# Optimization experiments

Hardware: AMD Instinct MI355X
Metric: run time of the kernel (lower is better)

Reference implementation:

```python
import jax, jax.numpy as jnp
import numpy as np


def _rule_stack(x_q):
    # x_q: [B, 2, 4]; a/b are the two context panels, per attribute column -> [B, 4]
    a = x_q[:, 0, :]
    b = x_q[:, 1, :]
    # 13 fixed rules applied elementwise across the 4 attribute columns -> [B, 4, 13]
    return jnp.stack([
        a,
        b - 2.0, b - 1.0, b + 1.0, b + 2.0,
        a - b, a + b,
        jnp.minimum(a, b), jnp.maximum(a, b),
        b + 2.0, b + 1.0, b - 2.0, b - 1.0,
    ], axis=-1)


def setup_inputs() -> dict:
    key = jax.random.key(0)
    k1, k2, k3, k4 = jax.random.split(key, 4)
    B, Z = 262144, 512
    z = jax.random.normal(k1, (B, Z), dtype=jnp.float32)
    x_q = jax.random.normal(k2, (B, 2, 4), dtype=jnp.float32)
    # rule_encoder: Linear(z_dim -> 4*13)
    W = jax.random.normal(k3, (Z, 52), dtype=jnp.float32) / np.sqrt(Z)
    b = jax.random.normal(k4, (52,), dtype=jnp.float32) * 0.01
    return {"z": z, "x_q": x_q, "W": W, "b": b}


def reference(z, x_q, W, b):
    logits = (z @ W + b).reshape(-1, 4, 13)          # [B, 4, 13]
    rule_probs = jax.nn.softmax(logits, axis=-1)       # [B, 4, 13]
    rules = _rule_stack(x_q)                           # [B, 4, 13]
    y_q = jnp.sum(rules * rule_probs, axis=-1)         # [B, 4]
    return y_q[:, None, :]                             # [B, 1, 4]
```

## Files before the change

kernel.cpp:

```cpp
#include <hip/hip_runtime.h>
#include <stdint.h>

typedef __bf16 bf16_t;
typedef bf16_t bf16x8 __attribute__((ext_vector_type(8)));
typedef float f32x4 __attribute__((ext_vector_type(4)));
typedef uint32_t u32x4 __attribute__((ext_vector_type(4)));
typedef uint16_t u16x8 __attribute__((ext_vector_type(8)));

union FragU { u32x4 u; bf16x8 v; u16x8 s; };

__device__ __forceinline__ uint16_t f2bf_rne(float f) {
  uint32_t u = __float_as_uint(f);
  return (uint16_t)((u + 0x7fffu + ((u >> 16) & 1u)) >> 16);
}
__device__ __forceinline__ float bf2f_bits(uint16_t h) {
  return __uint_as_float(((uint32_t)h) << 16);
}

__global__ __launch_bounds__(256) void pack_w_kernel(
    const float* __restrict__ W, u32x4* __restrict__ wf_hi,
    u32x4* __restrict__ wf_lo) {
  int idx = blockIdx.x * 256 + threadIdx.x;
  if (idx >= 4096) return;
  int lane = idx & 63;
  int nt   = (idx >> 6) & 3;
  int ks   = idx >> 8;
  int n  = nt * 16 + (lane & 15);
  int kb = ks * 32 + (lane >> 4) * 8;
  FragU hi, lo;
#pragma unroll
  for (int j = 0; j < 8; ++j) {
    float w = (n < 52) ? W[(kb + j) * 52 + n] : 0.0f;
    uint16_t h = f2bf_rne(w);
    hi.s[j] = h;
    lo.s[j] = f2bf_rne(w - bf2f_bits(h));
  }
  wf_hi[idx] = hi.u;
  wf_lo[idx] = lo.u;
}

#define MFMA16(a, b, c) __builtin_amdgcn_mfma_f32_16x16x32_bf16((a), (b), (c), 0, 0, 0)

__global__ __launch_bounds__(256, 3) void raven_main_kernel(
    const float* __restrict__ z, const float* __restrict__ xq,
    const u32x4* __restrict__ wfh, const u32x4* __restrict__ wfl,
    const float* __restrict__ bias, float* __restrict__ out) {
  __shared__ __align__(16) unsigned char smem[33280];
  __shared__ float lds_bias[52];

  const int tid  = threadIdx.x;
  const int wave = tid >> 6;
  const int lane = tid & 63;
  const int r  = lane & 15;
  const int kg = lane >> 4;

  if (tid < 52) lds_bias[tid] = bias[tid];

  const long long brow = (long long)blockIdx.x * 128;
  const long long wrow = brow + (long long)wave * 32;
  const float* zb = z + wrow * 512;

  unsigned char* stg = smem + wave * 8192;

  const int rloc = lane >> 3;
  const int foff = 4 * ((lane & 7) ^ rloc);

  f32x4 acc[2][4];
#pragma unroll
  for (int mt = 0; mt < 2; ++mt)
#pragma unroll
    for (int nt = 0; nt < 4; ++nt) {
      f32x4 zv = {0.0f, 0.0f, 0.0f, 0.0f};
      acc[mt][nt] = zv;
    }

#define STAGE_CHUNK(ks_, buf_)                                                  \
  {                                                                             \
    const float* g_ = zb + rloc * 512 + (ks_) * 32 + foff;                      \
    _Pragma("unroll")                                                           \
    for (int i_ = 0; i_ < 4; ++i_)                                              \
      __builtin_amdgcn_global_load_lds(                                         \
          (const __attribute__((address_space(1))) void*)(g_ + i_ * 8 * 512),   \
          (__attribute__((address_space(3))) void*)((buf_) + i_ * 1024),        \
          16, 0, 0);                                                            \
  }

  STAGE_CHUNK(0, stg);

  const int swz = (r & 7) << 4;

#pragma unroll
  for (int ks = 0; ks < 16; ++ks) {
    unsigned char* cur = stg + (ks & 1) * 4096;
    unsigned char* nxt = stg + ((ks + 1) & 1) * 4096;

    FragU bh[4], bl[4];
    const u32x4* ph = wfh + ks * 256 + lane;
    const u32x4* pl = wfl + ks * 256 + lane;
#pragma unroll
    for (int nt = 0; nt < 4; ++nt) {
      bh[nt].u = ph[nt * 64];
      bl[nt].u = pl[nt * 64];
    }
    __builtin_amdgcn_sched_barrier(0);

    if (ks < 15) STAGE_CHUNK(ks + 1, nxt);
    __builtin_amdgcn_sched_barrier(0);
    if (ks < 15) asm volatile("s_waitcnt vmcnt(4)" ::: "memory");
    else         asm volatile("s_waitcnt vmcnt(0)" ::: "memory");
    __builtin_amdgcn_sched_barrier(0);

    const unsigned char* c0 = cur + r * 128;
    const unsigned char* c1 = cur + (r + 16) * 128;
    f32x4 a00 = *(const f32x4*)(c0 + ((kg * 32) ^ swz));
    f32x4 a01 = *(const f32x4*)(c0 + ((kg * 32 + 16) ^ swz));
    f32x4 a10 = *(const f32x4*)(c1 + ((kg * 32) ^ swz));
    f32x4 a11 = *(const f32x4*)(c1 + ((kg * 32 + 16) ^ swz));

    FragU h0, h1;
#pragma unroll
    for (int j = 0; j < 4; ++j) {
      h0.v[j]     = (bf16_t)a00[j];
      h0.v[4 + j] = (bf16_t)a01[j];
      h1.v[j]     = (bf16_t)a10[j];
      h1.v[4 + j] = (bf16_t)a11[j];
    }

#pragma unroll
    for (int nt = 0; nt < 4; ++nt) {
      acc[0][nt] = MFMA16(h0.v, bh[nt].v, acc[0][nt]);
      acc[0][nt] = MFMA16(h0.v, bl[nt].v, acc[0][nt]);
      acc[1][nt] = MFMA16(h1.v, bh[nt].v, acc[1][nt]);
      acc[1][nt] = MFMA16(h1.v, bl[nt].v, acc[1][nt]);
    }
  }
#undef STAGE_CHUNK

  __syncthreads();

  float (*lds)[65] = (float(*)[65])smem;

#pragma unroll
  for (int mt = 0; mt < 2; ++mt)
#pragma unroll
    for (int nt = 0; nt < 4; ++nt)
#pragma unroll
      for (int i = 0; i < 4; ++i)
        lds[wave * 32 + mt * 16 + kg * 4 + i][nt * 16 + r] = acc[mt][nt][i];

  __syncthreads();

  for (int task = tid; task < 128 * 4; task += 256) {
    int row = task >> 2;
    int g   = task & 3;
    long long grow = brow + row;
    float a  = xq[grow * 8 + g];
    float bq = xq[grow * 8 + 4 + g];
    float l[13];
    float m = -1e30f;
#pragma unroll
    for (int u = 0; u < 13; ++u) {
      l[u] = lds[row][g * 13 + u] + lds_bias[g * 13 + u];
      m = fmaxf(m, l[u]);
    }
    float s = 0.0f;
#pragma unroll
    for (int u = 0; u < 13; ++u) {
      float e = __expf(l[u] - m);
      l[u] = e;
      s += e;
    }
    float num = a * l[0]
              + (bq - 2.0f) * (l[1] + l[11])
              + (bq - 1.0f) * (l[2] + l[12])
              + (bq + 1.0f) * (l[3] + l[10])
              + (bq + 2.0f) * (l[4] + l[9])
              + (a - bq) * l[5]
              + (a + bq) * l[6]
              + fminf(a, bq) * l[7]
              + fmaxf(a, bq) * l[8];
    out[grow * 4 + g] = num / s;
  }
}

extern "C" void kernel_launch(void* const* d_in, const int* in_sizes, int n_in,
                              void* d_out, int out_size, void* d_ws, size_t ws_size,
                              hipStream_t stream) {
  const float* z    = (const float*)d_in[0];
  const float* xq   = (const float*)d_in[1];
  const float* W    = (const float*)d_in[2];
  const float* bias = (const float*)d_in[3];
  float* out = (float*)d_out;

  const int B = in_sizes[0] / 512;

  u32x4* wf_hi = (u32x4*)d_ws;
  u32x4* wf_lo = wf_hi + 4096;

  hipLaunchKernelGGL(pack_w_kernel, dim3(16), dim3(256), 0, stream, W, wf_hi, wf_lo);

  const int blocks = B / 128;
  hipLaunchKernelGGL(raven_main_kernel, dim3(blocks), dim3(256), 0, stream,
                     z, xq, (const u32x4*)wf_hi, (const u32x4*)wf_lo, bias, out);
}
```

Baseline: 128.7 us.

## Deepen z staging to triple buffer and prefetch W fragments one step ahead

Moves the z LDS staging from double to triple buffering, so two chunks are in flight, and prefetches the W bf16 fragments for the next k-step into a second register set. Raises MFMA issue priority with s_setprio around the MFMA block. The epilogue now uses one thread per row with vectorized xq loads and a float4 store. The aim is to hide global memory latency in this bandwidth-bound GEMM. The cost is more LDS (48KB per block) and more registers, which may lower occupancy below the 3 blocks per CU requested in the launch bounds.

New measurement: 133.0 us. 3.4% more time.

```diff
diff --git a/kernel.cpp b/kernel.cpp
--- a/kernel.cpp
+++ b/kernel.cpp
@@ -45,7 +45,7 @@
     const float* __restrict__ z, const float* __restrict__ xq,
     const u32x4* __restrict__ wfh, const u32x4* __restrict__ wfl,
     const float* __restrict__ bias, float* __restrict__ out) {
-  __shared__ __align__(16) unsigned char smem[33280];
+  __shared__ __align__(16) unsigned char smem[49152];
   __shared__ float lds_bias[52];
 
   const int tid  = threadIdx.x;
@@ -60,7 +60,7 @@
   const long long wrow = brow + (long long)wave * 32;
   const float* zb = z + wrow * 512;
 
-  unsigned char* stg = smem + wave * 8192;
+  unsigned char* stg = smem + wave * 12288;
 
   const int rloc = lane >> 3;
   const int foff = 4 * ((lane & 7) ^ rloc);
@@ -85,29 +85,35 @@
           16, 0, 0);                                                            \
   }
 
+#define LOADB(ks_, set_)                                                        \
+  {                                                                             \
+    const u32x4* ph_ = wfh + (ks_) * 256 + lane;                                \
+    const u32x4* pl_ = wfl + (ks_) * 256 + lane;                                \
+    _Pragma("unroll")                                                           \
+    for (int nt_ = 0; nt_ < 4; ++nt_) {                                         \
+      bh[set_][nt_].u = ph_[nt_ * 64];                                          \
+      bl[set_][nt_].u = pl_[nt_ * 64];                                          \
+    }                                                                           \
+  }
+
+  FragU bh[2][4], bl[2][4];
+
   STAGE_CHUNK(0, stg);
+  STAGE_CHUNK(1, stg + 4096);
+  LOADB(0, 0);
 
   const int swz = (r & 7) << 4;
 
 #pragma unroll
   for (int ks = 0; ks < 16; ++ks) {
-    unsigned char* cur = stg + (ks & 1) * 4096;
-    unsigned char* nxt = stg + ((ks + 1) & 1) * 4096;
-
-    FragU bh[4], bl[4];
-    const u32x4* ph = wfh + ks * 256 + lane;
-    const u32x4* pl = wfl + ks * 256 + lane;
-#pragma unroll
-    for (int nt = 0; nt < 4; ++nt) {
-      bh[nt].u = ph[nt * 64];
-      bl[nt].u = pl[nt * 64];
-    }
+    unsigned char* cur = stg + (ks % 3) * 4096;
+
+    if (ks < 14) { unsigned char* n2 = stg + ((ks + 2) % 3) * 4096; STAGE_CHUNK(ks + 2, n2); }
+    if (ks < 15) LOADB(ks + 1, (ks + 1) & 1);
     __builtin_amdgcn_sched_barrier(0);
-
-    if (ks < 15) STAGE_CHUNK(ks + 1, nxt);
-    __builtin_amdgcn_sched_barrier(0);
-    if (ks < 15) asm volatile("s_waitcnt vmcnt(4)" ::: "memory");
-    else         asm volatile("s_waitcnt vmcnt(0)" ::: "memory");
+    if (ks < 14)      asm volatile("s_waitcnt vmcnt(12)" ::: "memory");
+    else if (ks == 14) asm volatile("s_waitcnt vmcnt(8)" ::: "memory");
+    else               asm volatile("s_waitcnt vmcnt(0)" ::: "memory");
     __builtin_amdgcn_sched_barrier(0);
 
     const unsigned char* c0 = cur + r * 128;
@@ -126,15 +132,19 @@
       h1.v[4 + j] = (bf16_t)a11[j];
     }
 
+    const int cs = ks & 1;
+    __builtin_amdgcn_s_setprio(1);
 #pragma unroll
     for (int nt = 0; nt < 4; ++nt) {
-      acc[0][nt] = MFMA16(h0.v, bh[nt].v, acc[0][nt]);
-      acc[0][nt] = MFMA16(h0.v, bl[nt].v, acc[0][nt]);
-      acc[1][nt] = MFMA16(h1.v, bh[nt].v, acc[1][nt]);
-      acc[1][nt] = MFMA16(h1.v, bl[nt].v, acc[1][nt]);
-    }
+      acc[0][nt] = MFMA16(h0.v, bh[cs][nt].v, acc[0][nt]);
+      acc[0][nt] = MFMA16(h0.v, bl[cs][nt].v, acc[0][nt]);
+      acc[1][nt] = MFMA16(h1.v, bh[cs][nt].v, acc[1][nt]);
+      acc[1][nt] = MFMA16(h1.v, bl[cs][nt].v, acc[1][nt]);
+    }
+    __builtin_amdgcn_s_setprio(0);
   }
 #undef STAGE_CHUNK
+#undef LOADB
 
   __syncthreads();
 
@@ -150,36 +160,42 @@
 
   __syncthreads();
 
-  for (int task = tid; task < 128 * 4; task += 256) {
-    int row = task >> 2;
-    int g   = task & 3;
+  if (tid < 128) {
+    int row = tid;
     long long grow = brow + row;
-    float a  = xq[grow * 8 + g];
-    float bq = xq[grow * 8 + 4 + g];
-    float l[13];
-    float m = -1e30f;
-#pragma unroll
-    for (int u = 0; u < 13; ++u) {
-      l[u] = lds[row][g * 13 + u] + lds_bias[g * 13 + u];
-      m = fmaxf(m, l[u]);
-    }
-    float s = 0.0f;
-#pragma unroll
-    for (int u = 0; u < 13; ++u) {
-      float e = __expf(l[u] - m);
-      l[u] = e;
-      s += e;
-    }
-    float num = a * l[0]
-              + (bq - 2.0f) * (l[1] + l[11])
-              + (bq - 1.0f) * (l[2] + l[12])
-              + (bq + 1.0f) * (l[3] + l[10])
-              + (bq + 2.0f) * (l[4] + l[9])
-              + (a - bq) * l[5]
-              + (a + bq) * l[6]
-              + fminf(a, bq) * l[7]
-              + fmaxf(a, bq) * l[8];
-    out[grow * 4 + g] = num / s;
+    f32x4 xa = *(const f32x4*)(xq + grow * 8);
+    f32x4 xb = *(const f32x4*)(xq + grow * 8 + 4);
+    f32x4 res;
+#pragma unroll
+    for (int g = 0; g < 4; ++g) {
+      float a  = xa[g];
+      float bq = xb[g];
+      float l[13];
+      float m = -1e30f;
+#pragma unroll
+      for (int u = 0; u < 13; ++u) {
+        l[u] = lds[row][g * 13 + u] + lds_bias[g * 13 + u];
+        m = fmaxf(m, l[u]);
+      }
+      float s = 0.0f;
+#pragma unroll
+      for (int u = 0; u < 13; ++u) {
+        float e = __expf(l[u] - m);
+        l[u] = e;
+        s += e;
+      }
+      float num = a * l[0]
+                + (bq - 2.0f) * (l[1] + l[11])
+                + (bq - 1.0f) * (l[2] + l[12])
+                + (bq + 1.0f) * (l[3] + l[10])
+                + (bq + 2.0f) * (l[4] + l[9])
+                + (a - bq) * l[5]
+                + (a + bq) * l[6]
+                + fminf(a, bq) * l[7]
+                + fmaxf(a, bq) * l[8];
+      res[g] = num / s;
+    }
+    *(f32x4*)(out + grow * 4) = res;
   }
 }
 
```

## Split K across waves with 32-row blocks and LDS atomic reduction

Applied to the files above, without the earlier changes.

Each block now handles 32 rows instead of 128. The four waves split the K dimension among themselves rather than each owning 32 rows. The z tile is staged in two half-K phases with block-wide barriers, and partial logits are combined through LDS atomicAdd before a 32-thread softmax/rule epilogue. The change raises the grid size and the occupancy target to spread memory traffic and latency. In exchange it drops the per-wave double-buffered pipelining, adds barriers and LDS atomics, and leaves most threads idle in the epilogue.

Result: slower. 337.4 us (+162.2%).

```diff
diff --git a/kernel.cpp b/kernel.cpp
--- a/kernel.cpp
+++ b/kernel.cpp
@@ -41,12 +41,11 @@
 
 #define MFMA16(a, b, c) __builtin_amdgcn_mfma_f32_16x16x32_bf16((a), (b), (c), 0, 0, 0)
 
-__global__ __launch_bounds__(256, 3) void raven_main_kernel(
+__global__ __launch_bounds__(256, 5) void raven_main_kernel(
     const float* __restrict__ z, const float* __restrict__ xq,
     const u32x4* __restrict__ wfh, const u32x4* __restrict__ wfl,
     const float* __restrict__ bias, float* __restrict__ out) {
-  __shared__ __align__(16) unsigned char smem[33280];
-  __shared__ float lds_bias[52];
+  __shared__ __align__(16) unsigned char smem[32768];
 
   const int tid  = threadIdx.x;
   const int wave = tid >> 6;
@@ -54,16 +53,8 @@
   const int r  = lane & 15;
   const int kg = lane >> 4;
 
-  if (tid < 52) lds_bias[tid] = bias[tid];
-
-  const long long brow = (long long)blockIdx.x * 128;
-  const long long wrow = brow + (long long)wave * 32;
-  const float* zb = z + wrow * 512;
-
-  unsigned char* stg = smem + wave * 8192;
-
-  const int rloc = lane >> 3;
-  const int foff = 4 * ((lane & 7) ^ rloc);
+  const long long brow = (long long)blockIdx.x * 32;
+  const float* zb = z + brow * 512;
 
   f32x4 acc[2][4];
 #pragma unroll
@@ -74,112 +65,121 @@
       acc[mt][nt] = zv;
     }
 
-#define STAGE_CHUNK(ks_, buf_)                                                  \
-  {                                                                             \
-    const float* g_ = zb + rloc * 512 + (ks_) * 32 + foff;                      \
-    _Pragma("unroll")                                                           \
-    for (int i_ = 0; i_ < 4; ++i_)                                              \
-      __builtin_amdgcn_global_load_lds(                                         \
-          (const __attribute__((address_space(1))) void*)(g_ + i_ * 8 * 512),   \
-          (__attribute__((address_space(3))) void*)((buf_) + i_ * 1024),        \
-          16, 0, 0);                                                            \
-  }
-
-  STAGE_CHUNK(0, stg);
-
-  const int swz = (r & 7) << 4;
-
-#pragma unroll
-  for (int ks = 0; ks < 16; ++ks) {
-    unsigned char* cur = stg + (ks & 1) * 4096;
-    unsigned char* nxt = stg + ((ks + 1) & 1) * 4096;
-
-    FragU bh[4], bl[4];
-    const u32x4* ph = wfh + ks * 256 + lane;
-    const u32x4* pl = wfl + ks * 256 + lane;
-#pragma unroll
-    for (int nt = 0; nt < 4; ++nt) {
-      bh[nt].u = ph[nt * 64];
-      bl[nt].u = pl[nt * 64];
-    }
-    __builtin_amdgcn_sched_barrier(0);
-
-    if (ks < 15) STAGE_CHUNK(ks + 1, nxt);
-    __builtin_amdgcn_sched_barrier(0);
-    if (ks < 15) asm volatile("s_waitcnt vmcnt(4)" ::: "memory");
-    else         asm volatile("s_waitcnt vmcnt(0)" ::: "memory");
-    __builtin_amdgcn_sched_barrier(0);
-
-    const unsigned char* c0 = cur + r * 128;
-    const unsigned char* c1 = cur + (r + 16) * 128;
-    f32x4 a00 = *(const f32x4*)(c0 + ((kg * 32) ^ swz));
-    f32x4 a01 = *(const f32x4*)(c0 + ((kg * 32 + 16) ^ swz));
-    f32x4 a10 = *(const f32x4*)(c1 + ((kg * 32) ^ swz));
-    f32x4 a11 = *(const f32x4*)(c1 + ((kg * 32 + 16) ^ swz));
-
-    FragU h0, h1;
-#pragma unroll
-    for (int j = 0; j < 4; ++j) {
-      h0.v[j]     = (bf16_t)a00[j];
-      h0.v[4 + j] = (bf16_t)a01[j];
-      h1.v[j]     = (bf16_t)a10[j];
-      h1.v[4 + j] = (bf16_t)a11[j];
-    }
-
-#pragma unroll
-    for (int nt = 0; nt < 4; ++nt) {
-      acc[0][nt] = MFMA16(h0.v, bh[nt].v, acc[0][nt]);
-      acc[0][nt] = MFMA16(h0.v, bl[nt].v, acc[0][nt]);
-      acc[1][nt] = MFMA16(h1.v, bh[nt].v, acc[1][nt]);
-      acc[1][nt] = MFMA16(h1.v, bl[nt].v, acc[1][nt]);
-    }
-  }
-#undef STAGE_CHUNK
-
+  const int lfo = lane * 4;
+  const int sw  = (r & 7) << 4;
+
+#pragma unroll
+  for (int p = 0; p < 2; ++p) {
+#pragma unroll
+    for (int i = 0; i < 8; ++i) {
+      const int row = wave * 8 + i;
+      const float* src = zb + row * 512 + p * 256 + (lfo ^ ((row & 7) * 4));
+      __builtin_amdgcn_global_load_lds(
+          (const __attribute__((address_space(1))) void*)src,
+          (__attribute__((address_space(3))) void*)(smem + row * 1024),
+          16, 0, 0);
+    }
+    __syncthreads();
+
+    const int kbase = p * 8 + wave * 2;
+#pragma unroll
+    for (int c = 0; c < 2; ++c) {
+      const int ksg = kbase + c;
+      FragU bh[4], bl[4];
+      const u32x4* ph = wfh + ksg * 256 + lane;
+      const u32x4* pl = wfl + ksg * 256 + lane;
+#pragma unroll
+      for (int nt = 0; nt < 4; ++nt) {
+        bh[nt].u = ph[nt * 64];
+        bl[nt].u = pl[nt * 64];
+      }
+
+      const int colb = (wave * 2 + c) * 128 + kg * 32;
+      const unsigned char* c0 = smem + r * 1024;
+      const unsigned char* c1 = smem + (r + 16) * 1024;
+      f32x4 a00 = *(const f32x4*)(c0 + ((colb     ) ^ sw));
+      f32x4 a01 = *(const f32x4*)(c0 + ((colb + 16) ^ sw));
+      f32x4 a10 = *(const f32x4*)(c1 + ((colb     ) ^ sw));
+      f32x4 a11 = *(const f32x4*)(c1 + ((colb + 16) ^ sw));
+
+      FragU h0, h1;
+#pragma unroll
+      for (int j = 0; j < 4; ++j) {
+        h0.v[j]     = (bf16_t)a00[j];
+        h0.v[4 + j] = (bf16_t)a01[j];
+        h1.v[j]     = (bf16_t)a10[j];
+        h1.v[4 + j] = (bf16_t)a11[j];
+      }
+
+#pragma unroll
+      for (int nt = 0; nt < 4; ++nt) {
+        acc[0][nt] = MFMA16(h0.v, bh[nt].v, acc[0][nt]);
+        acc[0][nt] = MFMA16(h0.v, bl[nt].v, acc[0][nt]);
+        acc[1][nt] = MFMA16(h1.v, bh[nt].v, acc[1][nt]);
+        acc[1][nt] = MFMA16(h1.v, bl[nt].v, acc[1][nt]);
+      }
+    }
+    __syncthreads();
+  }
+
+  float (*logits)[65] = (float(*)[65])smem;
+  if (wave == 0) {
+#pragma unroll
+    for (int mt = 0; mt < 2; ++mt)
+#pragma unroll
+      for (int nt = 0; nt < 4; ++nt)
+#pragma unroll
+        for (int i = 0; i < 4; ++i)
+          logits[mt * 16 + kg * 4 + i][nt * 16 + r] = acc[mt][nt][i];
+  }
   __syncthreads();
-
-  float (*lds)[65] = (float(*)[65])smem;
-
-#pragma unroll
-  for (int mt = 0; mt < 2; ++mt)
-#pragma unroll
-    for (int nt = 0; nt < 4; ++nt)
-#pragma unroll
-      for (int i = 0; i < 4; ++i)
-        lds[wave * 32 + mt * 16 + kg * 4 + i][nt * 16 + r] = acc[mt][nt][i];
-
+  if (wave != 0) {
+#pragma unroll
+    for (int mt = 0; mt < 2; ++mt)
+#pragma unroll
+      for (int nt = 0; nt < 4; ++nt)
+#pragma unroll
+        for (int i = 0; i < 4; ++i)
+          atomicAdd(&logits[mt * 16 + kg * 4 + i][nt * 16 + r], acc[mt][nt][i]);
+  }
   __syncthreads();
 
-  for (int task = tid; task < 128 * 4; task += 256) {
-    int row = task >> 2;
-    int g   = task & 3;
-    long long grow = brow + row;
-    float a  = xq[grow * 8 + g];
-    float bq = xq[grow * 8 + 4 + g];
-    float l[13];
-    float m = -1e30f;
-#pragma unroll
-    for (int u = 0; u < 13; ++u) {
-      l[u] = lds[row][g * 13 + u] + lds_bias[g * 13 + u];
-      m = fmaxf(m, l[u]);
-    }
-    float s = 0.0f;
-#pragma unroll
-    for (int u = 0; u < 13; ++u) {
-      float e = __expf(l[u] - m);
-      l[u] = e;
-      s += e;
-    }
-    float num = a * l[0]
-              + (bq - 2.0f) * (l[1] + l[11])
-              + (bq - 1.0f) * (l[2] + l[12])
-              + (bq + 1.0f) * (l[3] + l[10])
-              + (bq + 2.0f) * (l[4] + l[9])
-              + (a - bq) * l[5]
-              + (a + bq) * l[6]
-              + fminf(a, bq) * l[7]
-              + fmaxf(a, bq) * l[8];
-    out[grow * 4 + g] = num / s;
+  if (tid < 32) {
+    const int row = tid;
+    const long long grow = brow + row;
+    f32x4 xa = *(const f32x4*)(xq + grow * 8);
+    f32x4 xb = *(const f32x4*)(xq + grow * 8 + 4);
+    f32x4 res;
+#pragma unroll
+    for (int g = 0; g < 4; ++g) {
+      float a  = xa[g];
+      float bq = xb[g];
+      float l[13];
+      float m = -1e30f;
+#pragma unroll
+      for (int u = 0; u < 13; ++u) {
+        l[u] = logits[row][g * 13 + u] + bias[g * 13 + u];
+        m = fmaxf(m, l[u]);
+      }
+      float s = 0.0f;
+#pragma unroll
+      for (int u = 0; u < 13; ++u) {
+        float e = __expf(l[u] - m);
+        l[u] = e;
+        s += e;
+      }
+      float num = a * l[0]
+                + (bq - 2.0f) * (l[1] + l[11])
+                + (bq - 1.0f) * (l[2] + l[12])
+                + (bq + 1.0f) * (l[3] + l[10])
+                + (bq + 2.0f) * (l[4] + l[9])
+                + (a - bq) * l[5]
+                + (a + bq) * l[6]
+                + fminf(a, bq) * l[7]
+                + fmaxf(a, bq) * l[8];
+      res[g] = num / s;
+    }
+    *(f32x4*)(out + grow * 4) = res;
   }
 }
 
@@ -199,7 +199,7 @@
 
   hipLaunchKernelGGL(pack_w_kernel, dim3(16), dim3(256), 0, stream, W, wf_hi, wf_lo);
 
-  const int blocks = B / 128;
+  const int blocks = B / 32;
   hipLaunchKernelGGL(raven_main_kernel, dim3(blocks), dim3(256), 0, stream,
                      z, xq, (const u32x4*)wf_hi, (const u32x4*)wf_lo, bias, out);
 }
```
